# Kernel tuning notes

Hardware: AMD Instinct MI355X
Metric: run time of the kernel (lower is better)

## Reference

```python
import jax, jax.numpy as jnp
import numpy as np

B, S, D, H = 2, 2048, 2048, 16
NEG = -1e9


def setup_inputs() -> dict:
    key = jax.random.key(0)
    ks = jax.random.split(key, 5)
    x = jax.random.normal(ks[0], (B, S, D), dtype=jnp.float32)
    # additive causal mask: 0 on/below diagonal, -1e9 above
    causal = jnp.triu(jnp.full((S, S), NEG, dtype=jnp.float32), k=1)
    attn_mask = causal[None, None, :, :]  # [1,1,S,S]
    scale = 0.02
    Wq = jax.random.normal(ks[1], (D, D), dtype=jnp.float32) * scale
    Wk = jax.random.normal(ks[2], (D, D), dtype=jnp.float32) * scale
    Wv = jax.random.normal(ks[3], (D, D), dtype=jnp.float32) * scale
    Wo = jax.random.normal(ks[4], (D, D), dtype=jnp.float32) * scale
    return {"x": x, "attn_mask": attn_mask, "Wq": Wq, "Wk": Wk, "Wv": Wv, "Wo": Wo}


def reference(x, attn_mask, Wq, Wk, Wv, Wo):
    b, s, hidden = x.shape
    d = hidden // H
    # torch nn.Linear: y = x @ W.T (no bias since bias=None)
    q = (x @ Wq.T).reshape(b, s, H, d).transpose(0, 2, 1, 3)  # [b,h,s,d]
    k = (x @ Wk.T).reshape(b, s, H, d).transpose(0, 2, 1, 3)
    v = (x @ Wv.T).reshape(b, s, H, d).transpose(0, 2, 1, 3)
    q = q * (1.0 / float(d) ** 0.5)
    att = jnp.einsum("bhqd,bhkd->bhqk", q, k) + attn_mask  # [b,h,s,s]
    att = jax.nn.softmax(att.astype(jnp.float32), axis=-1).astype(x.dtype)
    y = jnp.einsum("bhqk,bhkd->bhqd", att, v)
    y = y.transpose(0, 2, 1, 3).reshape(b, s, hidden)
    return y @ Wo.T
```

## Files before the change

kernel.cpp:

```cpp
#include <hip/hip_runtime.h>
#include <hip/hip_bf16.h>
#include <cstdint>
#include <cstddef>

typedef __bf16 bf16;
typedef __bf16 bf16x8 __attribute__((ext_vector_type(8)));
typedef __bf16 bf16x4 __attribute__((ext_vector_type(4)));
typedef float f32x4 __attribute__((ext_vector_type(4)));

static constexpr int BATCH = 2;
static constexpr int SEQ = 2048;
static constexpr int DMODEL = 2048;
static constexpr int NH = 16;
static constexpr int HD = 128;
static constexpr int MROWS = BATCH * SEQ;

#define GLOBAL_AS(p) ((const __attribute__((address_space(1))) void*)(p))
#define LDS_AS(p)    ((__attribute__((address_space(3))) void*)(p))

__global__ void cvt5_kernel(const float* __restrict__ x,
                            const float* __restrict__ wq, const float* __restrict__ wk,
                            const float* __restrict__ wv, const float* __restrict__ wo,
                            bf16* __restrict__ dst) {
  const int i = blockIdx.x * blockDim.x + threadIdx.x;
  const float* src;
  int local;
  if (i < 2097152) { src = x; local = i; }
  else {
    const int r = i - 2097152;
    const int w = r >> 20;
    local = r & 1048575;
    src = (w == 0) ? wq : (w == 1) ? wk : (w == 2) ? wv : wo;
  }
  float4 f = reinterpret_cast<const float4*>(src)[local];
  bf16x4 o;
  o.x = (bf16)f.x; o.y = (bf16)f.y; o.z = (bf16)f.z; o.w = (bf16)f.w;
  reinterpret_cast<bf16x4*>(dst)[i] = o;
}

template <int MAT>
__global__ __launch_bounds__(256, 4) void gemm_proj(
    const bf16* __restrict__ A, const bf16* __restrict__ W,
    bf16* __restrict__ O) {
  constexpr int Kd = DMODEL;
  __shared__ __align__(16) bf16 As[128][64];
  __shared__ __align__(16) bf16 Bs[128][64];
  const int n0 = blockIdx.x * 128;
  const int m0 = blockIdx.y * 128;
  const int tid = threadIdx.x;
  const int wave = tid >> 6;
  const int lane = tid & 63;
  const int quad = lane >> 4;
  const int l16 = lane & 15;
  const int wm = (wave >> 1) * 64;
  const int wn = (wave & 1) * 64;
  const int srow = lane >> 3;
  const int schunk = ((lane & 7) - srow) & 7;

  f32x4 acc[4][4] = {};
  for (int kt = 0; kt < Kd; kt += 64) {
#pragma unroll
    for (int i = 0; i < 4; i++) {
      const int r = wave * 32 + i * 8;
      __builtin_amdgcn_global_load_lds(
          GLOBAL_AS(&A[(size_t)(m0 + r + srow) * Kd + kt + schunk * 8]),
          LDS_AS(&As[r][0]), 16, 0, 0);
      __builtin_amdgcn_global_load_lds(
          GLOBAL_AS(&W[(size_t)(n0 + r + srow) * Kd + kt + schunk * 8]),
          LDS_AS(&Bs[r][0]), 16, 0, 0);
    }
    __syncthreads();
#pragma unroll
    for (int ks = 0; ks < 2; ks++) {
      const int col = (((ks * 4 + quad + l16) & 7)) * 8;
      bf16x8 af[4], bfr[4];
#pragma unroll
      for (int t = 0; t < 4; t++)
        af[t] = *reinterpret_cast<const bf16x8*>(&As[wm + t * 16 + l16][col]);
#pragma unroll
      for (int t = 0; t < 4; t++)
        bfr[t] = *reinterpret_cast<const bf16x8*>(&Bs[wn + t * 16 + l16][col]);
#pragma unroll
      for (int tm = 0; tm < 4; tm++)
#pragma unroll
        for (int tn = 0; tn < 4; tn++)
          acc[tm][tn] = __builtin_amdgcn_mfma_f32_16x16x32_bf16(af[tm], bfr[tn], acc[tm][tn], 0, 0, 0);
    }
    __syncthreads();
  }
#pragma unroll
  for (int tm = 0; tm < 4; tm++) {
#pragma unroll
    for (int tn = 0; tn < 4; tn++) {
      const int row0 = m0 + wm + tm * 16 + quad * 4;
      const int col = n0 + wn + tn * 16 + l16;
      const int h = col >> 7, dd = col & 127;
      if constexpr (MAT == 2) {
        const int b = row0 >> 11, s = row0 & 2047;
        bf16x4 pk;
#pragma unroll
        for (int j = 0; j < 4; j++) pk[j] = (bf16)acc[tm][tn][j];
        *reinterpret_cast<bf16x4*>(&O[((size_t)(b * NH + h) * HD + dd) * SEQ + s]) = pk;
      } else {
        const float scale = (MAT == 0) ? 0.08838834764831845f : 1.0f;
#pragma unroll
        for (int j = 0; j < 4; j++) {
          const int row = row0 + j;
          const int b = row >> 11, s = row & 2047;
          O[((size_t)(b * NH + h) * SEQ + s) * HD + dd] = (bf16)(acc[tm][tn][j] * scale);
        }
      }
    }
  }
}

__global__ __launch_bounds__(256, 4) void gemm_out(
    const bf16* __restrict__ A, const bf16* __restrict__ W,
    float* __restrict__ Oout) {
  constexpr int Kd = DMODEL;
  __shared__ __align__(16) bf16 As[128][64];
  __shared__ __align__(16) bf16 Bs[128][64];
  const int n0 = blockIdx.x * 128;
  const int m0 = blockIdx.y * 128;
  const int tid = threadIdx.x;
  const int wave = tid >> 6;
  const int lane = tid & 63;
  const int quad = lane >> 4;
  const int l16 = lane & 15;
  const int wm = (wave >> 1) * 64;
  const int wn = (wave & 1) * 64;
  const int srow = lane >> 3;
  const int schunk = ((lane & 7) - srow) & 7;

  f32x4 acc[4][4] = {};
  for (int kt = 0; kt < Kd; kt += 64) {
#pragma unroll
    for (int i = 0; i < 4; i++) {
      const int r = wave * 32 + i * 8;
      __builtin_amdgcn_global_load_lds(
          GLOBAL_AS(&A[(size_t)(m0 + r + srow) * Kd + kt + schunk * 8]),
          LDS_AS(&As[r][0]), 16, 0, 0);
      __builtin_amdgcn_global_load_lds(
          GLOBAL_AS(&W[(size_t)(n0 + r + srow) * Kd + kt + schunk * 8]),
          LDS_AS(&Bs[r][0]), 16, 0, 0);
    }
    __syncthreads();
#pragma unroll
    for (int ks = 0; ks < 2; ks++) {
      const int col = (((ks * 4 + quad + l16) & 7)) * 8;
      bf16x8 af[4], bfr[4];
#pragma unroll
      for (int t = 0; t < 4; t++)
        af[t] = *reinterpret_cast<const bf16x8*>(&As[wm + t * 16 + l16][col]);
#pragma unroll
      for (int t = 0; t < 4; t++)
        bfr[t] = *reinterpret_cast<const bf16x8*>(&Bs[wn + t * 16 + l16][col]);
#pragma unroll
      for (int tm = 0; tm < 4; tm++)
#pragma unroll
        for (int tn = 0; tn < 4; tn++)
          acc[tm][tn] = __builtin_amdgcn_mfma_f32_16x16x32_bf16(af[tm], bfr[tn], acc[tm][tn], 0, 0, 0);
    }
    __syncthreads();
  }
#pragma unroll
  for (int tm = 0; tm < 4; tm++) {
#pragma unroll
    for (int tn = 0; tn < 4; tn++) {
      const int row0 = m0 + wm + tm * 16 + quad * 4;
      const int col = n0 + wn + tn * 16 + l16;
#pragma unroll
      for (int j = 0; j < 4; j++)
        Oout[(size_t)(row0 + j) * DMODEL + col] = acc[tm][tn][j];
    }
  }
}

__global__ __launch_bounds__(256, 2) void attn_kernel(
    const bf16* __restrict__ Q, const bf16* __restrict__ K,
    const bf16* __restrict__ Vt, bf16* __restrict__ Y) {
  const int j = blockIdx.x;
  const int bh = blockIdx.y;
  __shared__ __align__(16) char smem[74752];
  auto Ks0 = (bf16(*)[128])(smem);
  auto Ks1 = (bf16(*)[128])(smem + 16384);
  auto Vt0 = (bf16(*)[64])(smem + 32768);
  auto Vt1 = (bf16(*)[64])(smem + 49152);
  auto Ps  = (bf16(*)[16][72])(smem + 65536);
  const int tid = threadIdx.x;
  const int wave = tid >> 6;
  const int lane = tid & 63;
  const int quad = lane >> 4;
  const int l16 = lane & 15;

  const bf16* Kbh = K + (size_t)bh * SEQ * HD;
  const bf16* Vbh = Vt + (size_t)bh * HD * SEQ;
  const int b = bh >> 4, h = bh & 15;

  const int krow = lane >> 4;
  const int vrow = lane >> 3;
  const int vchunk = ((lane & 7) - vrow) & 7;

  auto stageK = [&](int kt, bf16 (*Kd)[128]) {
#pragma unroll
    for (int i = 0; i < 4; i++) {
      const int rbase = wave * 16 + i * 4;
      const int r = rbase + krow;
      const int c = ((lane & 15) - krow - i * 4) & 15;
      __builtin_amdgcn_global_load_lds(
          GLOBAL_AS(&Kbh[(size_t)(kt + r) * HD + c * 8]), LDS_AS(&Kd[rbase][0]), 16, 0, 0);
    }
  };
  auto stageV = [&](int kt, bf16 (*Vd)[64]) {
#pragma unroll
    for (int i = 0; i < 4; i++) {
      const int rbase = wave * 32 + i * 8;
      const int r = rbase + vrow;
      __builtin_amdgcn_global_load_lds(
          GLOBAL_AS(&Vbh[(size_t)r * SEQ + kt + vchunk * 8]), LDS_AS(&Vd[rbase][0]), 16, 0, 0);
    }
  };

  for (int pass = 0; pass < 2; ++pass) {
    const int qt = pass ? (31 - j) : j;
    const int q0 = qt * 64;
    const int ntiles = qt + 1;

    const bf16* Qw = Q + ((size_t)bh * SEQ + q0 + wave * 16) * HD;
    bf16x8 qf[4];
#pragma unroll
    for (int kk = 0; kk < 4; kk++)
      qf[kk] = *reinterpret_cast<const bf16x8*>(&Qw[(size_t)l16 * HD + kk * 32 + quad * 8]);

    f32x4 oacc[8] = {};
    float m_i = -3.0e38f, l_i = 0.f;

    stageK(0, Ks0);
    stageV(0, Vt0);
    asm volatile("s_waitcnt vmcnt(0)" ::: "memory");
    __builtin_amdgcn_s_barrier();
    __builtin_amdgcn_sched_barrier(0);

    for (int t = 0; t < ntiles; ++t) {
      bf16 (*Ksc)[128] = (t & 1) ? Ks1 : Ks0;
      bf16 (*Vtc)[64]  = (t & 1) ? Vt1 : Vt0;
      if (t + 1 < ntiles) {
        bf16 (*Ksn)[128] = (t & 1) ? Ks0 : Ks1;
        bf16 (*Vtn)[64]  = (t & 1) ? Vt0 : Vt1;
        stageK((t + 1) * 64, Ksn);
        stageV((t + 1) * 64, Vtn);
      }

      f32x4 sacc[4] = {};
#pragma unroll
      for (int kk = 0; kk < 4; kk++) {
        const int kcol = (((kk * 4 + quad + l16) & 15)) * 8;
        bf16x8 ka[4];
#pragma unroll
        for (int mt = 0; mt < 4; mt++)
          ka[mt] = *reinterpret_cast<const bf16x8*>(&Ksc[mt * 16 + l16][kcol]);
#pragma unroll
        for (int mt = 0; mt < 4; mt++)
          sacc[mt] = __builtin_amdgcn_mfma_f32_16x16x32_bf16(ka[mt], qf[kk], sacc[mt], 0, 0, 0);
      }

      const int qg_loc = wave * 16 + l16;
      float mx = -3.0e38f;
      if (t == ntiles - 1) {
#pragma unroll
        for (int mt = 0; mt < 4; mt++)
#pragma unroll
          for (int jj = 0; jj < 4; jj++) {
            const int kg = mt * 16 + quad * 4 + jj;
            float v = (kg <= qg_loc) ? sacc[mt][jj] : -3.0e38f;
            sacc[mt][jj] = v;
            mx = fmaxf(mx, v);
          }
      } else {
#pragma unroll
        for (int mt = 0; mt < 4; mt++)
#pragma unroll
          for (int jj = 0; jj < 4; jj++) mx = fmaxf(mx, sacc[mt][jj]);
      }
      mx = fmaxf(mx, __shfl_xor(mx, 16));
      mx = fmaxf(mx, __shfl_xor(mx, 32));
      const float mnew = fmaxf(m_i, mx);
      const float alpha = __expf(m_i - mnew);
      m_i = mnew;
      float rs = 0.f;
#pragma unroll
      for (int mt = 0; mt < 4; mt++)
#pragma unroll
        for (int jj = 0; jj < 4; jj++) {
          float p = __expf(sacc[mt][jj] - mnew);
          sacc[mt][jj] = p;
          rs += p;
        }
      rs += __shfl_xor(rs, 16);
      rs += __shfl_xor(rs, 32);
      l_i = l_i * alpha + rs;
#pragma unroll
      for (int mt8 = 0; mt8 < 8; mt8++)
#pragma unroll
        for (int jj = 0; jj < 4; jj++) oacc[mt8][jj] *= alpha;

#pragma unroll
      for (int mt = 0; mt < 4; mt++) {
        bf16x4 pk;
#pragma unroll
        for (int jj = 0; jj < 4; jj++) pk[jj] = (bf16)sacc[mt][jj];
        *reinterpret_cast<bf16x4*>(&Ps[wave][l16][mt * 16 + quad * 4]) = pk;
      }

#pragma unroll
      for (int kk2 = 0; kk2 < 2; kk2++) {
        const int vcol = ((kk2 * 4 + quad + l16) & 7) * 8;
        bf16x8 pb = *reinterpret_cast<const bf16x8*>(&Ps[wave][l16][kk2 * 32 + quad * 8]);
#pragma unroll
        for (int mt8 = 0; mt8 < 8; mt8++) {
          bf16x8 av = *reinterpret_cast<const bf16x8*>(&Vtc[mt8 * 16 + l16][vcol]);
          oacc[mt8] = __builtin_amdgcn_mfma_f32_16x16x32_bf16(av, pb, oacc[mt8], 0, 0, 0);
        }
      }

      asm volatile("s_waitcnt vmcnt(0)" ::: "memory");
      __builtin_amdgcn_s_barrier();
      __builtin_amdgcn_sched_barrier(0);
    }

    const float inv = 1.0f / l_i;
    const int qg = q0 + wave * 16 + l16;
#pragma unroll
    for (int mt8 = 0; mt8 < 8; mt8++) {
      bf16x4 pk;
#pragma unroll
      for (int jj = 0; jj < 4; jj++) pk[jj] = (bf16)(oacc[mt8][jj] * inv);
      *reinterpret_cast<bf16x4*>(
          &Y[(size_t)(b * SEQ + qg) * DMODEL + h * HD + mt8 * 16 + quad * 4]) = pk;
    }
  }
}

extern "C" void kernel_launch(void* const* d_in, const int* in_sizes, int n_in,
                              void* d_out, int out_size, void* d_ws, size_t ws_size,
                              hipStream_t stream) {
  const float* x  = (const float*)d_in[0];
  const float* Wq = (const float*)d_in[2];
  const float* Wk = (const float*)d_in[3];
  const float* Wv = (const float*)d_in[4];
  const float* Wo = (const float*)d_in[5];
  float* out = (float*)d_out;

  char* ws = (char*)d_ws;
  bf16* xb  = (bf16*)(ws + 0);
  bf16* Wqb = (bf16*)(ws + 16777216);
  bf16* Wkb = (bf16*)(ws + 25165824);
  bf16* Wvb = (bf16*)(ws + 33554432);
  bf16* Wob = (bf16*)(ws + 41943040);
  bf16* Qb  = (bf16*)(ws + 50331648);
  bf16* Kb  = (bf16*)(ws + 67108864);
  bf16* Vtb = (bf16*)(ws + 83886080);
  bf16* Yb  = xb;
  if (ws_size < 100663296) return;

  cvt5_kernel<<<24576, 256, 0, stream>>>(x, Wq, Wk, Wv, Wo, xb);

  gemm_proj<0><<<dim3(16, MROWS / 128), 256, 0, stream>>>(xb, Wqb, Qb);
  gemm_proj<1><<<dim3(16, MROWS / 128), 256, 0, stream>>>(xb, Wkb, Kb);
  gemm_proj<2><<<dim3(16, MROWS / 128), 256, 0, stream>>>(xb, Wvb, Vtb);

  attn_kernel<<<dim3(16, BATCH * NH), 256, 0, stream>>>(Qb, Kb, Vtb, Yb);

  gemm_out<<<dim3(16, MROWS / 128), 256, 0, stream>>>(
      Yb, Wob, out);
}
```

Baseline: 388.1 us.

## Fuse QKV projections, use 64-row out-proj tiles, XCD-aware attention block mapping

Merges the three Q/K/V projection GEMMs into one launch over the contiguous Wq/Wk/Wv bf16 buffer, choosing the output tensor per block from the column index. This removes two launches and gives a 768-block grid instead of three 256-block grids. The output projection now uses 64-row M tiles with higher occupancy bounds, so 512 blocks fill the CUs better. The attention grid is flattened and remapped so blocks sharing a batch-head land on the same XCD, which should improve L2 reuse of K and V. The trade-off is lower per-block arithmetic intensity in the output GEMM.

```diff
diff --git a/kernel.cpp b/kernel.cpp
--- a/kernel.cpp
+++ b/kernel.cpp
@@ -38,10 +38,9 @@
   reinterpret_cast<bf16x4*>(dst)[i] = o;
 }
 
-template <int MAT>
-__global__ __launch_bounds__(256, 4) void gemm_proj(
+__global__ __launch_bounds__(256, 4) void gemm_qkv(
     const bf16* __restrict__ A, const bf16* __restrict__ W,
-    bf16* __restrict__ O) {
+    bf16* __restrict__ Oq, bf16* __restrict__ Ok, bf16* __restrict__ Ov) {
   constexpr int Kd = DMODEL;
   __shared__ __align__(16) bf16 As[128][64];
   __shared__ __align__(16) bf16 Bs[128][64];
@@ -93,16 +92,18 @@
 #pragma unroll
     for (int tn = 0; tn < 4; tn++) {
       const int row0 = m0 + wm + tm * 16 + quad * 4;
-      const int col = n0 + wn + tn * 16 + l16;
+      const int mat = n0 >> 11;
+      const int col = (n0 & 2047) + wn + tn * 16 + l16;
       const int h = col >> 7, dd = col & 127;
-      if constexpr (MAT == 2) {
+      if (mat == 2) {
         const int b = row0 >> 11, s = row0 & 2047;
         bf16x4 pk;
 #pragma unroll
         for (int j = 0; j < 4; j++) pk[j] = (bf16)acc[tm][tn][j];
-        *reinterpret_cast<bf16x4*>(&O[((size_t)(b * NH + h) * HD + dd) * SEQ + s]) = pk;
+        *reinterpret_cast<bf16x4*>(&Ov[((size_t)(b * NH + h) * HD + dd) * SEQ + s]) = pk;
       } else {
-        const float scale = (MAT == 0) ? 0.08838834764831845f : 1.0f;
+        bf16* O = mat ? Ok : Oq;
+        const float scale = mat ? 1.0f : 0.08838834764831845f;
 #pragma unroll
         for (int j = 0; j < 4; j++) {
           const int row = row0 + j;
@@ -114,33 +115,37 @@
   }
 }
 
-__global__ __launch_bounds__(256, 4) void gemm_out(
+__global__ __launch_bounds__(256, 6) void gemm_out64(
     const bf16* __restrict__ A, const bf16* __restrict__ W,
     float* __restrict__ Oout) {
   constexpr int Kd = DMODEL;
-  __shared__ __align__(16) bf16 As[128][64];
+  __shared__ __align__(16) bf16 As[64][64];
   __shared__ __align__(16) bf16 Bs[128][64];
   const int n0 = blockIdx.x * 128;
-  const int m0 = blockIdx.y * 128;
+  const int m0 = blockIdx.y * 64;
   const int tid = threadIdx.x;
   const int wave = tid >> 6;
   const int lane = tid & 63;
   const int quad = lane >> 4;
   const int l16 = lane & 15;
-  const int wm = (wave >> 1) * 64;
+  const int wm = (wave >> 1) * 32;
   const int wn = (wave & 1) * 64;
   const int srow = lane >> 3;
   const int schunk = ((lane & 7) - srow) & 7;
 
-  f32x4 acc[4][4] = {};
+  f32x4 acc[2][4] = {};
   for (int kt = 0; kt < Kd; kt += 64) {
+#pragma unroll
+    for (int i = 0; i < 2; i++) {
+      const int r = wave * 16 + i * 8;
+      __builtin_amdgcn_global_load_lds(
+          GLOBAL_AS(&A[(size_t)(m0 + r + srow) * Kd + kt + schunk * 8]),
+          LDS_AS(&As[r][0]), 16, 0, 0);
+    }
 #pragma unroll
     for (int i = 0; i < 4; i++) {
       const int r = wave * 32 + i * 8;
       __builtin_amdgcn_global_load_lds(
-          GLOBAL_AS(&A[(size_t)(m0 + r + srow) * Kd + kt + schunk * 8]),
-          LDS_AS(&As[r][0]), 16, 0, 0);
-      __builtin_amdgcn_global_load_lds(
           GLOBAL_AS(&W[(size_t)(n0 + r + srow) * Kd + kt + schunk * 8]),
           LDS_AS(&Bs[r][0]), 16, 0, 0);
     }
@@ -148,15 +153,15 @@
 #pragma unroll
     for (int ks = 0; ks < 2; ks++) {
       const int col = (((ks * 4 + quad + l16) & 7)) * 8;
-      bf16x8 af[4], bfr[4];
-#pragma unroll
-      for (int t = 0; t < 4; t++)
+      bf16x8 af[2], bfr[4];
+#pragma unroll
+      for (int t = 0; t < 2; t++)
         af[t] = *reinterpret_cast<const bf16x8*>(&As[wm + t * 16 + l16][col]);
 #pragma unroll
       for (int t = 0; t < 4; t++)
         bfr[t] = *reinterpret_cast<const bf16x8*>(&Bs[wn + t * 16 + l16][col]);
 #pragma unroll
-      for (int tm = 0; tm < 4; tm++)
+      for (int tm = 0; tm < 2; tm++)
 #pragma unroll
         for (int tn = 0; tn < 4; tn++)
           acc[tm][tn] = __builtin_amdgcn_mfma_f32_16x16x32_bf16(af[tm], bfr[tn], acc[tm][tn], 0, 0, 0);
@@ -164,7 +169,7 @@
     __syncthreads();
   }
 #pragma unroll
-  for (int tm = 0; tm < 4; tm++) {
+  for (int tm = 0; tm < 2; tm++) {
 #pragma unroll
     for (int tn = 0; tn < 4; tn++) {
       const int row0 = m0 + wm + tm * 16 + quad * 4;
@@ -179,8 +184,11 @@
 __global__ __launch_bounds__(256, 2) void attn_kernel(
     const bf16* __restrict__ Q, const bf16* __restrict__ K,
     const bf16* __restrict__ Vt, bf16* __restrict__ Y) {
-  const int j = blockIdx.x;
-  const int bh = blockIdx.y;
+  const int lin = blockIdx.x;
+  const int xcd = lin & 7;
+  const int within = lin >> 3;
+  const int j = within & 15;
+  const int bh = xcd + 8 * (within >> 4);
   __shared__ __align__(16) char smem[74752];
   auto Ks0 = (bf16(*)[128])(smem);
   auto Ks1 = (bf16(*)[128])(smem + 16384);
@@ -354,8 +362,6 @@
   char* ws = (char*)d_ws;
   bf16* xb  = (bf16*)(ws + 0);
   bf16* Wqb = (bf16*)(ws + 16777216);
-  bf16* Wkb = (bf16*)(ws + 25165824);
-  bf16* Wvb = (bf16*)(ws + 33554432);
   bf16* Wob = (bf16*)(ws + 41943040);
   bf16* Qb  = (bf16*)(ws + 50331648);
   bf16* Kb  = (bf16*)(ws + 67108864);
@@ -365,12 +371,11 @@
 
   cvt5_kernel<<<24576, 256, 0, stream>>>(x, Wq, Wk, Wv, Wo, xb);
 
-  gemm_proj<0><<<dim3(16, MROWS / 128), 256, 0, stream>>>(xb, Wqb, Qb);
-  gemm_proj<1><<<dim3(16, MROWS / 128), 256, 0, stream>>>(xb, Wkb, Kb);
-  gemm_proj<2><<<dim3(16, MROWS / 128), 256, 0, stream>>>(xb, Wvb, Vtb);
-
-  attn_kernel<<<dim3(16, BATCH * NH), 256, 0, stream>>>(Qb, Kb, Vtb, Yb);
-
-  gemm_out<<<dim3(16, MROWS / 128), 256, 0, stream>>>(
+  gemm_qkv<<<dim3(48, MROWS / 128), 256, 0, stream>>>(
+      xb, Wqb, Qb, Kb, Vtb);
+
+  attn_kernel<<<512, 256, 0, stream>>>(Qb, Kb, Vtb, Yb);
+
+  gemm_out64<<<dim3(16, MROWS / 64), 256, 0, stream>>>(
       Yb, Wob, out);
 }
```

New measurement: 402.3 us. 3.7% more time.

## Fuse QKV projections into one launch and split-K the output projection

Applied to the files above, without the earlier changes.

The three Q/K/V projection GEMMs become a single launch with a 48-wide column grid. Each block works out which matrix it belongs to from its column offset and writes to the matching output, so there is one launch and a smaller partial last wave. The output projection is split in K into two halves, doubling the block count. Each half writes fp32 partials into freed workspace regions, and a separate reduce kernel sums them. The split-K path adds extra global memory traffic and one more launch, in exchange for better CU utilisation.

```diff
diff --git a/kernel.cpp b/kernel.cpp
--- a/kernel.cpp
+++ b/kernel.cpp
@@ -38,10 +38,9 @@
   reinterpret_cast<bf16x4*>(dst)[i] = o;
 }
 
-template <int MAT>
-__global__ __launch_bounds__(256, 4) void gemm_proj(
+__global__ __launch_bounds__(256, 4) void gemm_qkv(
     const bf16* __restrict__ A, const bf16* __restrict__ W,
-    bf16* __restrict__ O) {
+    bf16* __restrict__ Oq, bf16* __restrict__ Ok, bf16* __restrict__ Ov) {
   constexpr int Kd = DMODEL;
   __shared__ __align__(16) bf16 As[128][64];
   __shared__ __align__(16) bf16 Bs[128][64];
@@ -93,16 +92,18 @@
 #pragma unroll
     for (int tn = 0; tn < 4; tn++) {
       const int row0 = m0 + wm + tm * 16 + quad * 4;
-      const int col = n0 + wn + tn * 16 + l16;
+      const int mat = n0 >> 11;
+      const int col = (n0 & 2047) + wn + tn * 16 + l16;
       const int h = col >> 7, dd = col & 127;
-      if constexpr (MAT == 2) {
+      if (mat == 2) {
         const int b = row0 >> 11, s = row0 & 2047;
         bf16x4 pk;
 #pragma unroll
         for (int j = 0; j < 4; j++) pk[j] = (bf16)acc[tm][tn][j];
-        *reinterpret_cast<bf16x4*>(&O[((size_t)(b * NH + h) * HD + dd) * SEQ + s]) = pk;
+        *reinterpret_cast<bf16x4*>(&Ov[((size_t)(b * NH + h) * HD + dd) * SEQ + s]) = pk;
       } else {
-        const float scale = (MAT == 0) ? 0.08838834764831845f : 1.0f;
+        bf16* O = mat ? Ok : Oq;
+        const float scale = mat ? 1.0f : 0.08838834764831845f;
 #pragma unroll
         for (int j = 0; j < 4; j++) {
           const int row = row0 + j;
@@ -114,14 +115,14 @@
   }
 }
 
-__global__ __launch_bounds__(256, 4) void gemm_out(
+__global__ __launch_bounds__(256, 4) void gemm_out_sk(
     const bf16* __restrict__ A, const bf16* __restrict__ W,
-    float* __restrict__ Oout) {
-  constexpr int Kd = DMODEL;
+    float* __restrict__ P0, float* __restrict__ P1a, float* __restrict__ P1b) {
   __shared__ __align__(16) bf16 As[128][64];
   __shared__ __align__(16) bf16 Bs[128][64];
   const int n0 = blockIdx.x * 128;
   const int m0 = blockIdx.y * 128;
+  const int kz = blockIdx.z * 1024;
   const int tid = threadIdx.x;
   const int wave = tid >> 6;
   const int lane = tid & 63;
@@ -133,15 +134,15 @@
   const int schunk = ((lane & 7) - srow) & 7;
 
   f32x4 acc[4][4] = {};
-  for (int kt = 0; kt < Kd; kt += 64) {
+  for (int kt = kz; kt < kz + 1024; kt += 64) {
 #pragma unroll
     for (int i = 0; i < 4; i++) {
       const int r = wave * 32 + i * 8;
       __builtin_amdgcn_global_load_lds(
-          GLOBAL_AS(&A[(size_t)(m0 + r + srow) * Kd + kt + schunk * 8]),
+          GLOBAL_AS(&A[(size_t)(m0 + r + srow) * DMODEL + kt + schunk * 8]),
           LDS_AS(&As[r][0]), 16, 0, 0);
       __builtin_amdgcn_global_load_lds(
-          GLOBAL_AS(&W[(size_t)(n0 + r + srow) * Kd + kt + schunk * 8]),
+          GLOBAL_AS(&W[(size_t)(n0 + r + srow) * DMODEL + kt + schunk * 8]),
           LDS_AS(&Bs[r][0]), 16, 0, 0);
     }
     __syncthreads();
@@ -169,11 +170,33 @@
     for (int tn = 0; tn < 4; tn++) {
       const int row0 = m0 + wm + tm * 16 + quad * 4;
       const int col = n0 + wn + tn * 16 + l16;
-#pragma unroll
-      for (int j = 0; j < 4; j++)
-        Oout[(size_t)(row0 + j) * DMODEL + col] = acc[tm][tn][j];
-    }
-  }
+      if (blockIdx.z == 0) {
+#pragma unroll
+        for (int j = 0; j < 4; j++)
+          P0[(size_t)(row0 + j) * DMODEL + col] = acc[tm][tn][j];
+      } else if (row0 < 3072) {
+#pragma unroll
+        for (int j = 0; j < 4; j++)
+          P1a[(size_t)(row0 + j) * DMODEL + col] = acc[tm][tn][j];
+      } else {
+#pragma unroll
+        for (int j = 0; j < 4; j++)
+          P1b[(size_t)(row0 - 3072 + j) * DMODEL + col] = acc[tm][tn][j];
+      }
+    }
+  }
+}
+
+__global__ void reduce_out(const float* __restrict__ P0, const float* __restrict__ P1a,
+                           const float* __restrict__ P1b, float* __restrict__ out) {
+  const int i = blockIdx.x * blockDim.x + threadIdx.x;
+  const int e = i * 4;
+  const int row = e >> 11;
+  f32x4 a = *reinterpret_cast<const f32x4*>(&P0[e]);
+  f32x4 b = (row < 3072) ? *reinterpret_cast<const f32x4*>(&P1a[e])
+                         : *reinterpret_cast<const f32x4*>(&P1b[e - 3072 * 2048]);
+  f32x4 c = a + b;
+  *reinterpret_cast<f32x4*>(&out[e]) = c;
 }
 
 __global__ __launch_bounds__(256, 2) void attn_kernel(
@@ -354,23 +377,25 @@
   char* ws = (char*)d_ws;
   bf16* xb  = (bf16*)(ws + 0);
   bf16* Wqb = (bf16*)(ws + 16777216);
-  bf16* Wkb = (bf16*)(ws + 25165824);
-  bf16* Wvb = (bf16*)(ws + 33554432);
   bf16* Wob = (bf16*)(ws + 41943040);
   bf16* Qb  = (bf16*)(ws + 50331648);
   bf16* Kb  = (bf16*)(ws + 67108864);
   bf16* Vtb = (bf16*)(ws + 83886080);
   bf16* Yb  = xb;
+  float* P0  = (float*)(ws + 50331648);
+  float* P1a = (float*)(ws + 16777216);
+  float* P1b = (float*)(ws + 83886080);
   if (ws_size < 100663296) return;
 
   cvt5_kernel<<<24576, 256, 0, stream>>>(x, Wq, Wk, Wv, Wo, xb);
 
-  gemm_proj<0><<<dim3(16, MROWS / 128), 256, 0, stream>>>(xb, Wqb, Qb);
-  gemm_proj<1><<<dim3(16, MROWS / 128), 256, 0, stream>>>(xb, Wkb, Kb);
-  gemm_proj<2><<<dim3(16, MROWS / 128), 256, 0, stream>>>(xb, Wvb, Vtb);
+  gemm_qkv<<<dim3(48, MROWS / 128), 256, 0, stream>>>(
+      xb, Wqb, Qb, Kb, Vtb);
 
   attn_kernel<<<dim3(16, BATCH * NH), 256, 0, stream>>>(Qb, Kb, Vtb, Yb);
 
-  gemm_out<<<dim3(16, MROWS / 128), 256, 0, stream>>>(
-      Yb, Wob, out);
-}
+  gemm_out_sk<<<dim3(16, MROWS / 128, 2), 256, 0, stream>>>(
+      Yb, Wob, P0, P1a, P1b);
+
+  reduce_out<<<8192, 256, 0, stream>>>(P0, P1a, P1b, out);
+}
```

After: 381.0 us. No clear change (-1.8%).
